# Kernel optimization log

Hardware: AMD Instinct MI355X
Metric: run time of the kernel (lower is better)

## Reference

```python
import jax, jax.numpy as jnp
import numpy as np

H = 14
N = H * H
DIM = 768
INT = 5
LAM = 3.5


def fft_conv_grouped(x, w):
    # x: (B, g*in_c, N) real; w: (g, int_c, in_c, H, H//2+1) complex
    g, int_c, in_c = w.shape[:3]
    B = x.shape[0]
    xf = jnp.fft.rfftn(x.reshape(B, g, in_c, H, H), axes=(-2, -1), norm='ortho')
    yf = jnp.einsum('bgchf,gichf->bgihf', xf, w)
    y = jnp.fft.irfftn(yf, s=(H, H), axes=(-2, -1), norm='ortho')
    return y.reshape(B, g * int_c, N)


def soft(x, t):
    # sign(x) * relu(|x| - t)
    return jnp.sign(x) * jnp.maximum(jnp.abs(x) - t, 0.0)


def batch_norm(x, gamma, beta, eps=1e-5):
    # training-mode BatchNorm1d applied per channel over (B, N); x: (B, N, C)
    m = x.mean(axis=(0, 1))
    v = x.var(axis=(0, 1))
    return (x - m) * jax.lax.rsqrt(v + eps) * gamma + beta


def setup_inputs() -> dict:
    key = jax.random.key(0)
    ks = jax.random.split(key, 8)
    B = 32
    Hf = H // 2 + 1
    # kernel: init randn*0.06, then normalize_parameters()
    kr = jax.random.normal(ks[0], (DIM, INT, 1, H, Hf, 2), dtype=jnp.float32) * 0.06
    kc = kr[..., 0] + 1j * kr[..., 1]
    nrm = jnp.sqrt((jnp.abs(kc) ** 2).sum(axis=(2, 3, 4), keepdims=True) * 2.0 / H ** 2)
    kc = kc / nrm
    kernel = jnp.stack([jnp.real(kc), jnp.imag(kc)], axis=-1)
    # L buffer: update_L(lam=1) -> per-group max singular value of Gram kk
    kk = jnp.einsum('gichf,gjchf->gijhf', kc, jnp.conj(kc))
    sv = np.linalg.svd(np.asarray(jnp.transpose(kk, (0, 3, 4, 1, 2))), compute_uv=False)
    L = jnp.asarray(sv.reshape(DIM, -1).max(axis=-1), dtype=jnp.float32)
    hid = 4 * DIM
    return {
        'x': jax.random.normal(ks[1], (B, N, DIM), dtype=jnp.float32),
        'v_w': jax.random.normal(ks[2], (DIM, DIM), dtype=jnp.float32) * 0.02,
        'proj_w': jax.random.normal(ks[3], (DIM, DIM), dtype=jnp.float32) * 0.02,
        'proj_b': jnp.zeros((DIM,), dtype=jnp.float32),
        'kernel': kernel,
        'kernel2': jax.random.normal(ks[4], (DIM, 1, 1, H, Hf, 2), dtype=jnp.float32) * 0.02,
        'n1_g': jnp.ones((DIM,), dtype=jnp.float32),
        'n1_b': jnp.zeros((DIM,), dtype=jnp.float32),
        'n2_g': jnp.ones((DIM,), dtype=jnp.float32),
        'n2_b': jnp.zeros((DIM,), dtype=jnp.float32),
        'fc1_w': jax.random.normal(ks[5], (hid, DIM), dtype=jnp.float32) * 0.02,
        'fc1_b': jnp.zeros((hid,), dtype=jnp.float32),
        'fc2_w': jax.random.normal(ks[6], (DIM, hid), dtype=jnp.float32) * 0.02,
        'fc2_b': jnp.zeros((DIM,), dtype=jnp.float32),
        'L': L,
    }


def reference(x, v_w, proj_w, proj_b, kernel, kernel2, n1_g, n1_b, n2_g, n2_b, fc1_w, fc1_b, fc2_w, fc2_b, L):
    k = kernel[..., 0] + 1j * kernel[..., 1]                 # (g, int, 1, H, Hf)
    kk = jnp.einsum('gichf,gjchf->gijhf', k, jnp.conj(k))     # (g, int, int, H, Hf)
    vx = x @ v_w.T                                            # v Linear, no bias
    xc = jnp.swapaxes(vx, -2, -1)                             # (B, C, N)
    u = fft_conv_grouped(xc, k)                               # (B, g*int, N)
    Lv = jnp.repeat(L, INT)[None, :, None]                    # (1, g*int, 1)
    # ISTA: init soft-threshold then 3 gradient + shrink steps
    s = soft(u, LAM)
    for _ in range(3):
        s = s - (fft_conv_grouped(s, kk) - u) / Lv
        s = soft(s, LAM / Lv)
    # reconstruct with conjugate-transposed kernel, then mix with kernel2
    new = fft_conv_grouped(s, jnp.swapaxes(jnp.conj(k), 1, 2))  # (B, g, N)
    k2 = kernel2[..., 0] + 1j * kernel2[..., 1]
    new = fft_conv_grouped(new, k2)
    new = jnp.swapaxes(new, -2, -1)                           # (B, N, C)
    new = x + (batch_norm(new, n1_g, n1_b) @ proj_w.T + proj_b)
    h = jax.nn.gelu(batch_norm(new, n2_g, n2_b) @ fc1_w.T + fc1_b, approximate=False)
    return new + (h @ fc2_w.T + fc2_b)
```

## Files before the change

### kernel.cpp

```cpp
#include <hip/hip_runtime.h>
#include <cmath>

typedef unsigned short u16;
typedef __bf16 bf16x8 __attribute__((ext_vector_type(8)));
typedef float f32x4 __attribute__((ext_vector_type(4)));
typedef float float4v __attribute__((ext_vector_type(4)));
typedef u16 ushort4v __attribute__((ext_vector_type(4)));
typedef u16 ushort8v __attribute__((ext_vector_type(8)));

#define DIMC 768
#define NP 196
#define MTOT 6272
#define HIDC 3072
#define LAMC 3.5f

__device__ const float C14d[14] = {
  1.0f, 0.9009688679024191f, 0.6234898018587336f, 0.22252093395631445f,
  -0.22252093395631445f, -0.6234898018587336f, -0.9009688679024191f, -1.0f,
  -0.9009688679024191f, -0.6234898018587336f, -0.22252093395631445f,
  0.22252093395631445f, 0.6234898018587336f, 0.9009688679024191f
};
__device__ const float S14d[14] = {
  0.0f, 0.43388373911755823f, 0.7818314824680298f, 0.9749279121818236f,
  0.9749279121818236f, 0.7818314824680298f, 0.43388373911755823f, 0.0f,
  -0.43388373911755823f, -0.7818314824680298f, -0.9749279121818236f,
  -0.9749279121818236f, -0.7818314824680298f, -0.43388373911755823f
};

__device__ __forceinline__ u16 f2bf(float f) {
  unsigned u = __builtin_bit_cast(unsigned, f);
  unsigned r = u + 0x7FFFu + ((u >> 16) & 1u);
  return (u16)(r >> 16);
}

typedef const __attribute__((address_space(1))) u16* gas_p;
typedef __attribute__((address_space(3))) u16* las_p;
__device__ __forceinline__ void gl16(const u16* g, u16* l) {
  __builtin_amdgcn_global_load_lds((gas_p)g, (las_p)l, 16, 0, 0);
}

__global__ __launch_bounds__(256) void prep_k(
    const float* __restrict__ v_w, const float* __restrict__ fc2w,
    const float* __restrict__ x,
    u16* __restrict__ vwbf, u16* __restrict__ fc2bf, u16* __restrict__ xbf,
    u16* __restrict__ Ff, u16* __restrict__ Gf) {
  const int bid = blockIdx.x, t = threadIdx.x;
  if (bid < 378) {
    int idx = bid * 256 + t;
    if (idx < 50176) {
      int j = idx & 7, lane = (idx >> 3) & 63;
      int mk = idx >> 9, k0 = mk % 7, m0 = mk / 7;
      int s = m0 * 16 + (lane & 15);
      int q = k0 * 32 + (lane >> 4) * 8 + j;
      float v = 0.f;
      if (q < 196) {
        int kr = s >> 4, f = (s >> 1) & 7, r = q / 14, c = q % 14;
        int th = (kr * r + f * c) % 14;
        v = (s & 1) ? -S14d[th] : C14d[th];
      }
      Ff[idx] = f2bf(v);
    } else {
      int t2 = idx - 50176;
      int j = t2 & 7, lane = (t2 >> 3) & 63;
      int pk = t2 >> 9, k0 = pk % 7, p0 = pk / 7;
      int p = p0 * 16 + (lane & 15);
      int s = k0 * 32 + (lane >> 4) * 8 + j;
      float v = 0.f;
      if (p < 196) {
        int kr = s >> 4, f = (s >> 1) & 7, r = p / 14, c = p % 14;
        int th = (kr * r + f * c) % 14;
        float w = (f == 0 || f == 7) ? 1.f : 2.f;
        v = (w * (1.f / 196.f)) * ((s & 1) ? -S14d[th] : C14d[th]);
      }
      Gf[t2] = f2bf(v);
    }
  } else if (bid < 3258) {
    int idx = (bid - 378) * 256 + t;
    const float* s; u16* d; int base;
    if (idx < 147456) { s = v_w; d = vwbf; base = 0; }
    else              { s = fc2w; d = fc2bf; base = 147456; }
    int i4 = (idx - base) * 4;
    float4v v = *(const float4v*)(s + i4);
    ushort4v o;
#pragma unroll
    for (int j = 0; j < 4; ++j) o[j] = f2bf(v[j]);
    *(ushort4v*)(d + i4) = o;
  } else {
    int idx = (bid - 3258) * 256 + t;
    int i4 = idx * 4;
    float4v v = *(const float4v*)(x + i4);
    ushort4v o;
#pragma unroll
    for (int j = 0; j < 4; ++j) o[j] = f2bf(v[j]);
    *(ushort4v*)(xbf + i4) = o;
  }
}

template<int EPI>
__global__ __launch_bounds__(256) void gemm_k(
    const u16* __restrict__ A, const u16* __restrict__ Bw,
    const float* __restrict__ bias, const float* __restrict__ res,
    void* __restrict__ Cp, int Nr, int Kr, int ld, int NB) {
  __shared__ __attribute__((aligned(16))) u16 As[128 * 32];
  __shared__ __attribute__((aligned(16))) u16 Bs[128 * 32];
  const int t = threadIdx.x;
  const int wid = t >> 6, lane = t & 63;

  const int bid = blockIdx.x;
  const int xcd = bid & 7, j = bid >> 3;
  const int bmi = xcd + 8 * (j / NB);
  if (bmi >= 49) return;
  const int bn = (j % NB) * 128, bm = bmi * 128;

  const int wm = (wid >> 1) * 64, wn = (wid & 1) * 64;
  const int l15 = lane & 15, l4 = lane >> 4;
  const int srow = lane >> 2;
  const int sw_s = ((lane >> 2) ^ (lane >> 4)) & 3;
  const int scol = ((lane & 3) ^ sw_s) * 8;
  const int sw_r = (l15 ^ (l15 >> 2)) & 3;
  const int rcol = (l4 ^ sw_r) * 8;

  f32x4 acc[4][4];
#pragma unroll
  for (int a = 0; a < 4; ++a)
#pragma unroll
    for (int b2 = 0; b2 < 4; ++b2) acc[a][b2] = (f32x4){0.f, 0.f, 0.f, 0.f};

  const u16* gA0 = A + (size_t)(bm + wid * 16 + srow) * ld + scol;
  const u16* gB0 = Bw + (size_t)(bn + wid * 16 + srow) * ld + scol;
  u16* lA = As + wid * 512;
  u16* lB = Bs + wid * 512;

  for (int k0 = 0; k0 < Kr; k0 += 32) {
    gl16(gA0 + k0, lA);
    gl16(gA0 + (size_t)64 * ld + k0, lA + 2048);
    gl16(gB0 + k0, lB);
    gl16(gB0 + (size_t)64 * ld + k0, lB + 2048);
    __syncthreads();

    bf16x8 af[4], bfv[4];
#pragma unroll
    for (int mb = 0; mb < 4; ++mb)
      af[mb] = *(const bf16x8*)&As[(wm + mb * 16 + l15) * 32 + rcol];
#pragma unroll
    for (int nb = 0; nb < 4; ++nb)
      bfv[nb] = *(const bf16x8*)&Bs[(wn + nb * 16 + l15) * 32 + rcol];
#pragma unroll
    for (int mb = 0; mb < 4; ++mb)
#pragma unroll
      for (int nb = 0; nb < 4; ++nb)
        acc[mb][nb] = __builtin_amdgcn_mfma_f32_16x16x32_bf16(af[mb], bfv[nb], acc[mb][nb], 0, 0, 0);
    __syncthreads();
  }

#pragma unroll
  for (int mb = 0; mb < 4; ++mb) {
#pragma unroll
    for (int nb = 0; nb < 4; ++nb) {
      int n = bn + wn + nb * 16 + l15;
      if (EPI == 0) {
        int m0 = bm + wm + mb * 16 + l4 * 4;
        int bb = m0 / 196, np0 = m0 - bb * 196;
        *(float4v*)&((float*)Cp)[((size_t)bb * DIMC + n) * 196 + np0] =
            (float4v){acc[mb][nb][0], acc[mb][nb][1], acc[mb][nb][2], acc[mb][nb][3]};
      } else {
#pragma unroll
        for (int r = 0; r < 4; ++r) {
          int m = bm + wm + mb * 16 + l4 * 4 + r;
          float v = acc[mb][nb][r];
          if (EPI == 1) {
            ((float*)Cp)[(size_t)m * Nr + n] = v + bias[n] + res[(size_t)m * Nr + n];
          } else {
            float vb = v + bias[n];
            float ge = 0.5f * vb * (1.f + erff(vb * 0.70710678118654752f));
            ((u16*)Cp)[(size_t)m * Nr + n] = f2bf(ge);
          }
        }
      }
    }
  }
}

__global__ __launch_bounds__(64) void checkmfma_k(
    const float* __restrict__ vxt, const float* __restrict__ kern,
    const u16* __restrict__ Ff, const u16* __restrict__ Gf,
    int* __restrict__ cnt, int* __restrict__ wl) {
  __shared__ float xf[16 * 228];
  const int lane = threadIdx.x;
  const int wgb = blockIdx.x;
  const int g = wgb >> 1, bhalf = wgb & 1;
  const int tl = lane & 15, h = lane >> 4;
  const float* xbase = vxt + ((size_t)(bhalf * 16 + tl) * DIMC + g) * 196;

  bf16x8 Bx[7];
#pragma unroll
  for (int k0 = 0; k0 < 7; ++k0) {
    int q0 = k0 * 32 + h * 8;
    ushort8v tv;
    if (k0 < 6) {
      float4v f0 = *(const float4v*)(xbase + q0);
      float4v f1 = *(const float4v*)(xbase + q0 + 4);
#pragma unroll
      for (int j = 0; j < 4; ++j) { tv[j] = f2bf(f0[j]); tv[j + 4] = f2bf(f1[j]); }
    } else {
#pragma unroll
      for (int j = 0; j < 8; ++j) {
        int q = q0 + j;
        tv[j] = (q < 196) ? f2bf(xbase[q]) : (u16)0;
      }
    }
    Bx[k0] = __builtin_bit_cast(bf16x8, tv);
  }

  for (int m0 = 0; m0 < 14; ++m0) {
    f32x4 acc = (f32x4){0.f, 0.f, 0.f, 0.f};
#pragma unroll
    for (int k0 = 0; k0 < 7; ++k0) {
      bf16x8 Af = __builtin_bit_cast(bf16x8,
          *(const ushort8v*)(Ff + ((size_t)(m0 * 7 + k0) * 64 + lane) * 8));
      acc = __builtin_amdgcn_mfma_f32_16x16x32_bf16(Af, Bx[k0], acc, 0, 0, 0);
    }
    *(f32x4*)&xf[tl * 228 + m0 * 16 + h * 4] = acc;
  }

  bf16x8 By[5][7];
#pragma unroll
  for (int i = 0; i < 5; ++i) {
    const float* kb = kern + ((size_t)g * 5 + i) * 224;
#pragma unroll
    for (int k0 = 0; k0 < 7; ++k0) {
      f32x4 x0 = *(const f32x4*)&xf[tl * 228 + k0 * 32 + h * 8];
      f32x4 x1 = *(const f32x4*)&xf[tl * 228 + k0 * 32 + h * 8 + 4];
      int mb = k0 * 16 + h * 4;
      float2 ka = *(const float2*)(kb + (mb + 0) * 2);
      float2 kc = *(const float2*)(kb + (mb + 1) * 2);
      float2 ke = *(const float2*)(kb + (mb + 2) * 2);
      float2 kg = *(const float2*)(kb + (mb + 3) * 2);
      ushort8v tv;
      tv[0] = f2bf(ka.x * x0[0] - ka.y * x0[1]);
      tv[1] = f2bf(ka.x * x0[1] + ka.y * x0[0]);
      tv[2] = f2bf(kc.x * x0[2] - kc.y * x0[3]);
      tv[3] = f2bf(kc.x * x0[3] + kc.y * x0[2]);
      tv[4] = f2bf(ke.x * x1[0] - ke.y * x1[1]);
      tv[5] = f2bf(ke.x * x1[1] + ke.y * x1[0]);
      tv[6] = f2bf(kg.x * x1[2] - kg.y * x1[3]);
      tv[7] = f2bf(kg.x * x1[3] + kg.y * x1[2]);
      By[i][k0] = __builtin_bit_cast(bf16x8, tv);
    }
  }

  float vmax = 0.f;
  for (int p0 = 0; p0 < 13; ++p0) {
    f32x4 a0 = (f32x4){0.f, 0.f, 0.f, 0.f};
    f32x4 a1 = a0, a2 = a0, a3 = a0, a4 = a0;
#pragma unroll
    for (int k0 = 0; k0 < 7; ++k0) {
      bf16x8 Ag = __builtin_bit_cast(bf16x8,
          *(const ushort8v*)(Gf + ((size_t)(p0 * 7 + k0) * 64 + lane) * 8));
      a0 = __builtin_amdgcn_mfma_f32_16x16x32_bf16(Ag, By[0][k0], a0, 0, 0, 0);
      a1 = __builtin_amdgcn_mfma_f32_16x16x32_bf16(Ag, By[1][k0], a1, 0, 0, 0);
      a2 = __builtin_amdgcn_mfma_f32_16x16x32_bf16(Ag, By[2][k0], a2, 0, 0, 0);
      a3 = __builtin_amdgcn_mfma_f32_16x16x32_bf16(Ag, By[3][k0], a3, 0, 0, 0);
      a4 = __builtin_amdgcn_mfma_f32_16x16x32_bf16(Ag, By[4][k0], a4, 0, 0, 0);
    }
#pragma unroll
    for (int r = 0; r < 4; ++r) {
      vmax = fmaxf(vmax, fabsf(a0[r]));
      vmax = fmaxf(vmax, fabsf(a1[r]));
      vmax = fmaxf(vmax, fabsf(a2[r]));
      vmax = fmaxf(vmax, fabsf(a3[r]));
      vmax = fmaxf(vmax, fabsf(a4[r]));
    }
  }
  vmax = fmaxf(vmax, __shfl_xor(vmax, 16));
  vmax = fmaxf(vmax, __shfl_xor(vmax, 32));
  if (lane < 16 && vmax > (LAMC - 0.1f)) {
    int idx = atomicAdd(cnt, 1);
    wl[idx] = g * 32 + bhalf * 16 + lane;
  }
}

__global__ __launch_bounds__(64) void slow_k(
    const float* __restrict__ vxt, const float* __restrict__ kern,
    const float* __restrict__ kern2, const float* __restrict__ Lbuf,
    const int* __restrict__ cnt, const int* __restrict__ wl,
    float* __restrict__ outp,
    float* __restrict__ tsum, float* __restrict__ tsq,
    unsigned* __restrict__ maskg, unsigned* __restrict__ bmask) {
  const int ntile = *cnt;
  if ((int)blockIdx.x >= ntile) return;
  const int t = threadIdx.x;
  __shared__ float TC[196], TSn[196];
  __shared__ float xs[196];
  __shared__ float t1R[112], t1I[112];
  __shared__ float t2R[112], t2I[112];
  __shared__ float zr[112], zi[112];
  __shared__ float kR[5][112], kI[5][112];
  __shared__ float uu[5][196];
  __shared__ float ss[5][196];
  __shared__ float k2R[112], k2I[112];

  for (int i = t; i < 196; i += 64) {
    int a = i / 14, c = i - (i / 14) * 14;
    int m = (a * c) % 14;
    TC[i] = C14d[m]; TSn[i] = S14d[m];
  }

  auto rowsFwd = [&](const float* xsrc) {
    for (int i = t; i < 112; i += 64) {
      int r = i >> 3, f = i & 7;
      const float* xp = xsrc + r * 14;
      const float* tc = &TC[f * 14]; const float* tsn = &TSn[f * 14];
      float ar = 0.f, ai = 0.f;
#pragma unroll
      for (int c = 0; c < 14; ++c) { float xv = xp[c]; ar += xv * tc[c]; ai -= xv * tsn[c]; }
      t1R[i] = ar; t1I[i] = ai;
    }
    __syncthreads();
  };
  auto colsFwd = [&](float* oR, float* oI) {
    for (int i = t; i < 112; i += 64) {
      int kr = i >> 3, f = i & 7;
      const float* tc = &TC[kr * 14]; const float* tsn = &TSn[kr * 14];
      float br = 0.f, bi = 0.f;
#pragma unroll
      for (int r = 0; r < 14; ++r) {
        float xr = t1R[r * 8 + f], xi = t1I[r * 8 + f];
        br += tc[r] * xr + tsn[r] * xi;
        bi += tc[r] * xi - tsn[r] * xr;
      }
      oR[i] = br; oI[i] = bi;
    }
    __syncthreads();
  };
  auto colsInv = [&]() {
    for (int i = t; i < 112; i += 64) {
      int r = i >> 3, f = i & 7;
      const float* tc = &TC[r * 14]; const float* tsn = &TSn[r * 14];
      float br = 0.f, bi = 0.f;
#pragma unroll
      for (int kr = 0; kr < 14; ++kr) {
        float xr = t1R[kr * 8 + f], xi = t1I[kr * 8 + f];
        br += tc[kr] * xr - tsn[kr] * xi;
        bi += tc[kr] * xi + tsn[kr] * xr;
      }
      t2R[i] = br; t2I[i] = bi;
    }
    __syncthreads();
  };
  auto rowVal = [&](int r, int c) -> float {
    const float* pR = &t2R[r * 8]; const float* pI = &t2I[r * 8];
    float v = pR[0] + ((c & 1) ? -pR[7] : pR[7]);
    float s2 = 0.f;
#pragma unroll
    for (int f = 1; f < 7; ++f) s2 += pR[f] * TC[f * 14 + c] - pI[f] * TSn[f * 14 + c];
    return (v + 2.f * s2) * (1.0f / 196.0f);
  };

  for (int widx = blockIdx.x; widx < ntile; widx += gridDim.x) {
    const int tile = wl[widx];
    const int g = tile >> 5, b = tile & 31;
    __syncthreads();
    for (int i = t; i < 560; i += 64) {
      int ii = i / 112, p = i - ii * 112;
      const float* kp = kern + ((size_t)g * 5 + ii) * 224 + p * 2;
      kR[ii][p] = kp[0]; kI[ii][p] = kp[1];
    }
    for (int i = t; i < 196; i += 64) xs[i] = vxt[((size_t)b * DIMC + g) * 196 + i];
    for (int i = t; i < 112; i += 64) {
      k2R[i] = kern2[(size_t)g * 224 + i * 2];
      k2I[i] = kern2[(size_t)g * 224 + i * 2 + 1];
    }
    __syncthreads();

    rowsFwd(xs);
    colsFwd(zr, zi);
    for (int ii = 0; ii < 5; ++ii) {
      for (int i = t; i < 112; i += 64) {
        float a = kR[ii][i], b2 = kI[ii][i];
        t1R[i] = a * zr[i] - b2 * zi[i];
        t1I[i] = a * zi[i] + b2 * zr[i];
      }
      __syncthreads();
      colsInv();
      for (int i = t; i < 196; i += 64) uu[ii][i] = rowVal(i / 14, i - (i / 14) * 14);
      __syncthreads();
    }

    const float invL = 1.0f / Lbuf[g];
    const float thr = LAMC * invL;
    {
      float* up = &uu[0][0];
      float* sp = &ss[0][0];
      for (int i = t; i < 980; i += 64) {
        float v = up[i];
        float a = fabsf(v) - LAMC;
        sp[i] = a > 0.f ? copysignf(a, v) : 0.f;
      }
    }
    __syncthreads();

    for (int iter = 0; iter < 4; ++iter) {
      for (int i = t; i < 112; i += 64) { zr[i] = 0.f; zi[i] = 0.f; }
      __syncthreads();
      for (int ii = 0; ii < 5; ++ii) {
        rowsFwd(&ss[ii][0]);
        colsFwd(t2R, t2I);
        for (int i = t; i < 112; i += 64) {
          float a = kR[ii][i], b2 = kI[ii][i];
          zr[i] += a * t2R[i] + b2 * t2I[i];
          zi[i] += a * t2I[i] - b2 * t2R[i];
        }
        __syncthreads();
      }
      if (iter == 3) break;
      for (int ii = 0; ii < 5; ++ii) {
        for (int i = t; i < 112; i += 64) {
          float a = kR[ii][i], b2 = kI[ii][i];
          t1R[i] = a * zr[i] - b2 * zi[i];
          t1I[i] = a * zi[i] + b2 * zr[i];
        }
        __syncthreads();
        colsInv();
        for (int i = t; i < 196; i += 64) {
          float v = rowVal(i / 14, i - (i / 14) * 14);
          float sv = ss[ii][i] - (v - uu[ii][i]) * invL;
          float aa = fabsf(sv) - thr;
          ss[ii][i] = aa > 0.f ? copysignf(aa, sv) : 0.f;
        }
        __syncthreads();
      }
    }

    if (t < 28) {
      int kr = t >> 1, f = (t & 1) * 7;
      int d = kr * 8 + f;
      int srci = ((14 - kr) % 14) * 8 + f;
      float pr = 0.5f * (zr[d] + zr[srci]);
      float pi = 0.5f * (zi[d] - zi[srci]);
      zr[d] = pr; zi[d] = pi;
    }
    __syncthreads();
    for (int i = t; i < 112; i += 64) {
      float a = k2R[i], b2 = k2I[i];
      t1R[i] = a * zr[i] - b2 * zi[i];
      t1I[i] = a * zi[i] + b2 * zr[i];
    }
    __syncthreads();
    colsInv();
    float sacc = 0.f, qacc = 0.f;
    for (int i = t; i < 196; i += 64) {
      float v = rowVal(i / 14, i - (i / 14) * 14);
      outp[((size_t)(b * 196 + i)) * DIMC + g] = v;
      sacc += v; qacc += v * v;
    }
#pragma unroll
    for (int off = 32; off; off >>= 1) {
      sacc += __shfl_xor(sacc, off);
      qacc += __shfl_xor(qacc, off);
    }
    if (t == 0) {
      tsum[tile] = sacc; tsq[tile] = qacc;
      atomicOr(&maskg[g], 1u << b);
      atomicOr(bmask, 1u << b);
    }
  }
}

__global__ __launch_bounds__(256) void stats1c0_k(
    const float* __restrict__ tsum, const float* __restrict__ tsq,
    const unsigned* __restrict__ maskg,
    const float* __restrict__ gam, const float* __restrict__ bet,
    const float* __restrict__ projw, const float* __restrict__ pb,
    float* __restrict__ sc1, float* __restrict__ c0) {
  __shared__ float sh1s[768];
  const int t = threadIdx.x;
  for (int c = t; c < DIMC; c += 256) {
    unsigned mask = maskg[c];
    float S = 0.f, Q = 0.f;
    if (mask) {
      for (int b = 0; b < 32; ++b)
        if ((mask >> b) & 1) { S += tsum[c * 32 + b]; Q += tsq[c * 32 + b]; }
    }
    float m = S * (1.0f / 6272.0f);
    float v = fmaxf(Q * (1.0f / 6272.0f) - m * m, 0.f);
    float rs = rsqrtf(v + 1e-5f);
    float sc = gam[c] * rs;
    sh1s[c] = bet[c] - m * sc;
    if (blockIdx.x == 0) sc1[c] = sc;
  }
  __syncthreads();
  int n = blockIdx.x * 256 + t;
  const float* row = projw + (size_t)n * DIMC;
  float s = 0.f;
  for (int g = 0; g < DIMC; g += 4) {
    float4v r = *(const float4v*)(row + g);
    s += r[0] * sh1s[g] + r[1] * sh1s[g + 1] + r[2] * sh1s[g + 2] + r[3] * sh1s[g + 3];
  }
  c0[n] = s + pb[n];
}

__global__ __launch_bounds__(256) void bnb_k(
    const float* __restrict__ x, const float* __restrict__ c0,
    const float* __restrict__ sc1, const unsigned* __restrict__ maskg,
    const unsigned* __restrict__ bmask, const float* __restrict__ newm,
    const float* __restrict__ projw,
    float* __restrict__ new2, u16* __restrict__ n2bf,
    float* __restrict__ part) {
  const int jb = blockIdx.x, b = blockIdx.y, t = threadIdx.x;
  __shared__ unsigned gm[24];
  __shared__ float c0s[768];
  const bool hasb = ((*bmask >> b) & 1u) != 0u;
  if (t < 24) {
    unsigned w = 0;
    if (hasb)
      for (int j2 = 0; j2 < 32; ++j2) w |= ((maskg[t * 32 + j2] >> b) & 1u) << j2;
    gm[t] = w;
  }
  for (int c = t; c < 768; c += 256) c0s[c] = c0[c];
  __syncthreads();

  float S0 = 0, S1 = 0, S2 = 0, Q0 = 0, Q1 = 0, Q2 = 0;
  for (int mr = 0; mr < 7; ++mr) {
    size_t row = ((size_t)b * 196 + jb * 7 + mr) * DIMC;
#pragma unroll
    for (int j2 = 0; j2 < 3; ++j2) {
      int n = t + j2 * 256;
      float v = x[row + n] + c0s[n];
      if (hasb) {
        for (int w = 0; w < 24; ++w) {
          unsigned bits = gm[w];
          while (bits) {
            int g = w * 32 + __builtin_ctz(bits);
            bits &= bits - 1;
            v += sc1[g] * newm[row + g] * projw[(size_t)n * DIMC + g];
          }
        }
      }
      new2[row + n] = v;
      n2bf[row + n] = f2bf(v);
      if (j2 == 0) { S0 += v; Q0 += v * v; }
      else if (j2 == 1) { S1 += v; Q1 += v * v; }
      else { S2 += v; Q2 += v * v; }
    }
  }
  float* p = part + (size_t)(b * 28 + jb) * 1536;
  p[t] = S0; p[t + 256] = S1; p[t + 512] = S2;
  p[768 + t] = Q0; p[768 + 256 + t] = Q1; p[768 + 512 + t] = Q2;
}

__global__ __launch_bounds__(256) void red2_k(const float* __restrict__ part,
                                              float* __restrict__ part2) {
  int slot = blockIdx.x * 256 + threadIdx.x;
  int b = blockIdx.y;
  float s = 0.f;
  const float* p = part + (size_t)(b * 28) * 1536 + slot;
  for (int jb = 0; jb < 28; ++jb) s += p[(size_t)jb * 1536];
  part2[(size_t)b * 1536 + slot] = s;
}

__global__ __launch_bounds__(256) void stats2fin_k(const float* __restrict__ part2,
    const float* __restrict__ gam, const float* __restrict__ bet,
    float* __restrict__ scale, float* __restrict__ shift) {
  int c = blockIdx.x * 256 + threadIdx.x;
  float S = 0.f, Q = 0.f;
  for (int b = 0; b < 32; ++b) {
    S += part2[(size_t)b * 1536 + c];
    Q += part2[(size_t)b * 1536 + 768 + c];
  }
  float m = S * (1.0f / 6272.0f);
  float v = fmaxf(Q * (1.0f / 6272.0f) - m * m, 0.f);
  float rs = rsqrtf(v + 1e-5f);
  float sc = gam[c] * rs;
  scale[c] = sc;
  shift[c] = bet[c] - m * sc;
}

__global__ __launch_bounds__(256) void foldfc1_k(const float* __restrict__ fc1w,
    const float* __restrict__ fc1b, const float* __restrict__ sc2,
    const float* __restrict__ sh2, u16* __restrict__ fc1s,
    float* __restrict__ d0) {
  const int bid = blockIdx.x, t = threadIdx.x;
  if (bid < 12) {
    int n = bid * 256 + t;
    const float* row = fc1w + (size_t)n * DIMC;
    float s = 0.f;
    for (int k = 0; k < DIMC; k += 4) {
      float4v r = *(const float4v*)(row + k);
      float4v h = *(const float4v*)(sh2 + k);
      s += r[0] * h[0] + r[1] * h[1] + r[2] * h[2] + r[3] * h[3];
    }
    d0[n] = s + fc1b[n];
  } else {
    int idx = (bid - 12) * 256 + t;
    int i4 = idx * 4;
    int k = i4 % DIMC;
    float4v v = *(const float4v*)(fc1w + i4);
    float4v s = *(const float4v*)(sc2 + k);
    v = v * s;
    ushort4v o;
#pragma unroll
    for (int j = 0; j < 4; ++j) o[j] = f2bf(v[j]);
    *(ushort4v*)(fc1s + i4) = o;
  }
}

extern "C" void kernel_launch(void* const* d_in, const int* in_sizes, int n_in,
                              void* d_out, int out_size, void* d_ws, size_t ws_size,
                              hipStream_t stream) {
  (void)in_sizes; (void)n_in; (void)out_size;
  const float* x      = (const float*)d_in[0];
  const float* v_w    = (const float*)d_in[1];
  const float* proj_w = (const float*)d_in[2];
  const float* proj_b = (const float*)d_in[3];
  const float* kern   = (const float*)d_in[4];
  const float* kern2  = (const float*)d_in[5];
  const float* n1g    = (const float*)d_in[6];
  const float* n1b    = (const float*)d_in[7];
  const float* n2g    = (const float*)d_in[8];
  const float* n2b    = (const float*)d_in[9];
  const float* fc1w   = (const float*)d_in[10];
  const float* fc1b   = (const float*)d_in[11];
  const float* fc2w   = (const float*)d_in[12];
  const float* fc2b   = (const float*)d_in[13];
  const float* Lb     = (const float*)d_in[14];
  float* out = (float*)d_out;

  char* ws = (char*)d_ws;
  size_t o = 0;
  auto alloc = [&](size_t bytes) { size_t r = o; o += (bytes + 255) & ~(size_t)255; return r; };
  u16*   vwbf   = (u16*)(ws + alloc(589824 * 2));
  u16*   fc2bf  = (u16*)(ws + alloc(2359296 * 2));
  u16*   fc1s   = (u16*)(ws + alloc(2359296 * 2));
  u16*   Ffb    = (u16*)(ws + alloc(50176 * 2));
  u16*   Gfb    = (u16*)(ws + alloc(46592 * 2));
  float* sc1    = (float*)(ws + alloc(768 * 4));
  float* sc2    = (float*)(ws + alloc(768 * 4));
  float* sh2    = (float*)(ws + alloc(768 * 4));
  float* c0     = (float*)(ws + alloc(768 * 4));
  float* d0     = (float*)(ws + alloc(3072 * 4));
  float* part   = (float*)(ws + alloc((size_t)896 * 1536 * 4));
  float* part2  = (float*)(ws + alloc((size_t)32 * 1536 * 4));
  char*  zblk   = (char*)(ws + alloc(4096));
  int*      cnt   = (int*)zblk;
  unsigned* bmask = (unsigned*)(zblk + 4);
  unsigned* maskg = (unsigned*)(zblk + 8);
  int*   wl     = (int*)(ws + alloc(24576 * 4));
  float* tsum   = (float*)(ws + alloc(24576 * 4));
  float* tsq    = (float*)(ws + alloc(24576 * 4));
  u16*   xbf    = (u16*)(ws + alloc((size_t)MTOT * DIMC * 2));
  u16*   n2bf   = (u16*)(ws + alloc((size_t)MTOT * DIMC * 2));
  float* vxt    = (float*)(ws + alloc((size_t)MTOT * DIMC * 4));
  float* newm   = (float*)(ws + alloc((size_t)MTOT * DIMC * 4));
  float* new2   = (float*)(ws + alloc((size_t)MTOT * DIMC * 4));
  u16*   hbf    = (u16*)vxt;
  if (ws_size < o) return;

  hipMemsetAsync(zblk, 0, 4096, stream);

  prep_k<<<7962, 256, 0, stream>>>(v_w, fc2w, x, vwbf, fc2bf, xbf, Ffb, Gfb);
  gemm_k<0><<<336, 256, 0, stream>>>(xbf, vwbf, nullptr, nullptr, vxt, DIMC, DIMC, DIMC, 6);
  checkmfma_k<<<1536, 64, 0, stream>>>(vxt, kern, Ffb, Gfb, cnt, wl);
  slow_k<<<1024, 64, 0, stream>>>(vxt, kern, kern2, Lb, cnt, wl, newm,
                                  tsum, tsq, maskg, bmask);
  stats1c0_k<<<3, 256, 0, stream>>>(tsum, tsq, maskg, n1g, n1b, proj_w, proj_b, sc1, c0);
  bnb_k<<<dim3(28, 32), 256, 0, stream>>>(x, c0, sc1, maskg, bmask, newm, proj_w,
                                          new2, n2bf, part);
  red2_k<<<dim3(6, 32), 256, 0, stream>>>(part, part2);
  stats2fin_k<<<3, 256, 0, stream>>>(part2, n2g, n2b, sc2, sh2);
  foldfc1_k<<<2316, 256, 0, stream>>>(fc1w, fc1b, sc2, sh2, fc1s, d0);
  gemm_k<2><<<1344, 256, 0, stream>>>(n2bf, fc1s, d0, nullptr, hbf, HIDC, DIMC, DIMC, 24);
  gemm_k<1><<<336, 256, 0, stream>>>(hbf, fc2bf, fc2b, new2, out, DIMC, HIDC, HIDC, 6);
}
```

Measured before the change: 305.8 us.

## Pre-swizzle GEMM operands into MFMA fragment layout and drop LDS staging

All bf16 GEMM operands (x, v_w, fc2_w, folded fc1_w, the n2 activations and the GELU output) are now written in a 16x32-chunk fragment layout. Each lane can then load its MFMA operand straight from global memory with one 16-byte load. The GEMM kernel drops shared memory and __syncthreads. Each wave now computes its own 64x64 tile, with the block covering 64 rows by 256 columns. This removes LDS traffic and barriers, but operands are no longer shared between waves through LDS, so global/L2 reads increase and there is no explicit prefetch.

```diff
diff --git a/kernel.cpp b/kernel.cpp
--- a/kernel.cpp
+++ b/kernel.cpp
@@ -33,16 +33,15 @@
   return (u16)(r >> 16);
 }
 
-typedef const __attribute__((address_space(1))) u16* gas_p;
-typedef __attribute__((address_space(3))) u16* las_p;
-__device__ __forceinline__ void gl16(const u16* g, u16* l) {
-  __builtin_amdgcn_global_load_lds((gas_p)g, (las_p)l, 16, 0, 0);
+__device__ __forceinline__ size_t fidx(int m, int k, int K) {
+  return ((size_t)(m >> 4) * (K >> 5) + (k >> 5)) * 512 +
+         (size_t)((((k >> 3) & 3) * 16 + (m & 15)) * 8 + (k & 7));
 }
 
 __global__ __launch_bounds__(256) void prep_k(
     const float* __restrict__ v_w, const float* __restrict__ fc2w,
     const float* __restrict__ x,
-    u16* __restrict__ vwbf, u16* __restrict__ fc2bf, u16* __restrict__ xbf,
+    u16* __restrict__ vwf, u16* __restrict__ fc2f, u16* __restrict__ xf,
     u16* __restrict__ Ff, u16* __restrict__ Gf) {
   const int bid = blockIdx.x, t = threadIdx.x;
   if (bid < 378) {
@@ -74,51 +73,42 @@
       }
       Gf[t2] = f2bf(v);
     }
-  } else if (bid < 3258) {
-    int idx = (bid - 378) * 256 + t;
-    const float* s; u16* d; int base;
-    if (idx < 147456) { s = v_w; d = vwbf; base = 0; }
-    else              { s = fc2w; d = fc2bf; base = 147456; }
-    int i4 = (idx - base) * 4;
-    float4v v = *(const float4v*)(s + i4);
-    ushort4v o;
-#pragma unroll
-    for (int j = 0; j < 4; ++j) o[j] = f2bf(v[j]);
-    *(ushort4v*)(d + i4) = o;
-  } else {
-    int idx = (bid - 3258) * 256 + t;
-    int i4 = idx * 4;
-    float4v v = *(const float4v*)(x + i4);
-    ushort4v o;
-#pragma unroll
-    for (int j = 0; j < 4; ++j) o[j] = f2bf(v[j]);
-    *(ushort4v*)(xbf + i4) = o;
-  }
+    return;
+  }
+  const float* src; u16* dst; int idx, K;
+  if (bid < 666)        { src = v_w;  dst = vwf;  idx = (bid - 378) * 256 + t;  K = DIMC; }
+  else if (bid < 1818)  { src = fc2w; dst = fc2f; idx = (bid - 666) * 256 + t;  K = HIDC; }
+  else                  { src = x;    dst = xf;   idx = (bid - 1818) * 256 + t; K = DIMC; }
+  const int KC = K >> 5;
+  int chunk = idx >> 6, l = idx & 63;
+  int row = (chunk / KC) * 16 + (l & 15);
+  int k0 = (chunk % KC) * 32 + (l >> 4) * 8;
+  const float* sp = src + (size_t)row * K + k0;
+  float4v f0 = *(const float4v*)sp;
+  float4v f1 = *(const float4v*)(sp + 4);
+  ushort8v o;
+#pragma unroll
+  for (int j = 0; j < 4; ++j) { o[j] = f2bf(f0[j]); o[j + 4] = f2bf(f1[j]); }
+  *(ushort8v*)(dst + (size_t)idx * 8) = o;
 }
 
 template<int EPI>
-__global__ __launch_bounds__(256) void gemm_k(
-    const u16* __restrict__ A, const u16* __restrict__ Bw,
+__global__ __launch_bounds__(256) void gemmw_k(
+    const u16* __restrict__ Af, const u16* __restrict__ Bf,
     const float* __restrict__ bias, const float* __restrict__ res,
-    void* __restrict__ Cp, int Nr, int Kr, int ld, int NB) {
-  __shared__ __attribute__((aligned(16))) u16 As[128 * 32];
-  __shared__ __attribute__((aligned(16))) u16 Bs[128 * 32];
-  const int t = threadIdx.x;
-  const int wid = t >> 6, lane = t & 63;
-
+    void* __restrict__ Cp, int Nr, int Kr, int NB) {
+  const int t = threadIdx.x, w = t >> 6, lane = t & 63;
   const int bid = blockIdx.x;
   const int xcd = bid & 7, j = bid >> 3;
-  const int bmi = xcd + 8 * (j / NB);
-  if (bmi >= 49) return;
-  const int bn = (j % NB) * 128, bm = bmi * 128;
-
-  const int wm = (wid >> 1) * 64, wn = (wid & 1) * 64;
+  const int mt = xcd + 8 * (j / NB);
+  if (mt >= 98) return;
+  const int m0 = mt * 64;
+  const int n0 = ((j % NB) * 4 + w) * 64;
+  const int KC = Kr >> 5;
   const int l15 = lane & 15, l4 = lane >> 4;
-  const int srow = lane >> 2;
-  const int sw_s = ((lane >> 2) ^ (lane >> 4)) & 3;
-  const int scol = ((lane & 3) ^ sw_s) * 8;
-  const int sw_r = (l15 ^ (l15 >> 2)) & 3;
-  const int rcol = (l4 ^ sw_r) * 8;
+
+  const u16* Ab = Af + ((size_t)(m0 >> 4) * KC) * 512 + lane * 8;
+  const u16* Bb = Bf + ((size_t)(n0 >> 4) * KC) * 512 + lane * 8;
 
   f32x4 acc[4][4];
 #pragma unroll
@@ -126,54 +116,42 @@
 #pragma unroll
     for (int b2 = 0; b2 < 4; ++b2) acc[a][b2] = (f32x4){0.f, 0.f, 0.f, 0.f};
 
-  const u16* gA0 = A + (size_t)(bm + wid * 16 + srow) * ld + scol;
-  const u16* gB0 = Bw + (size_t)(bn + wid * 16 + srow) * ld + scol;
-  u16* lA = As + wid * 512;
-  u16* lB = Bs + wid * 512;
-
-  for (int k0 = 0; k0 < Kr; k0 += 32) {
-    gl16(gA0 + k0, lA);
-    gl16(gA0 + (size_t)64 * ld + k0, lA + 2048);
-    gl16(gB0 + k0, lB);
-    gl16(gB0 + (size_t)64 * ld + k0, lB + 2048);
-    __syncthreads();
-
+  for (int kc = 0; kc < KC; ++kc) {
     bf16x8 af[4], bfv[4];
 #pragma unroll
     for (int mb = 0; mb < 4; ++mb)
-      af[mb] = *(const bf16x8*)&As[(wm + mb * 16 + l15) * 32 + rcol];
+      af[mb] = *(const bf16x8*)(Ab + ((size_t)mb * KC + kc) * 512);
 #pragma unroll
     for (int nb = 0; nb < 4; ++nb)
-      bfv[nb] = *(const bf16x8*)&Bs[(wn + nb * 16 + l15) * 32 + rcol];
+      bfv[nb] = *(const bf16x8*)(Bb + ((size_t)nb * KC + kc) * 512);
 #pragma unroll
     for (int mb = 0; mb < 4; ++mb)
 #pragma unroll
       for (int nb = 0; nb < 4; ++nb)
         acc[mb][nb] = __builtin_amdgcn_mfma_f32_16x16x32_bf16(af[mb], bfv[nb], acc[mb][nb], 0, 0, 0);
-    __syncthreads();
   }
 
 #pragma unroll
   for (int mb = 0; mb < 4; ++mb) {
 #pragma unroll
     for (int nb = 0; nb < 4; ++nb) {
-      int n = bn + wn + nb * 16 + l15;
+      int n = n0 + nb * 16 + l15;
       if (EPI == 0) {
-        int m0 = bm + wm + mb * 16 + l4 * 4;
-        int bb = m0 / 196, np0 = m0 - bb * 196;
+        int m0r = m0 + mb * 16 + l4 * 4;
+        int bb = m0r / 196, np0 = m0r - bb * 196;
         *(float4v*)&((float*)Cp)[((size_t)bb * DIMC + n) * 196 + np0] =
             (float4v){acc[mb][nb][0], acc[mb][nb][1], acc[mb][nb][2], acc[mb][nb][3]};
       } else {
 #pragma unroll
         for (int r = 0; r < 4; ++r) {
-          int m = bm + wm + mb * 16 + l4 * 4 + r;
+          int m = m0 + mb * 16 + l4 * 4 + r;
           float v = acc[mb][nb][r];
           if (EPI == 1) {
             ((float*)Cp)[(size_t)m * Nr + n] = v + bias[n] + res[(size_t)m * Nr + n];
           } else {
             float vb = v + bias[n];
             float ge = 0.5f * vb * (1.f + erff(vb * 0.70710678118654752f));
-            ((u16*)Cp)[(size_t)m * Nr + n] = f2bf(ge);
+            ((u16*)Cp)[fidx(m, n, Nr)] = f2bf(ge);
           }
         }
       }
@@ -505,7 +483,7 @@
     const float* __restrict__ sc1, const unsigned* __restrict__ maskg,
     const unsigned* __restrict__ bmask, const float* __restrict__ newm,
     const float* __restrict__ projw,
-    float* __restrict__ new2, u16* __restrict__ n2bf,
+    float* __restrict__ new2, u16* __restrict__ n2f,
     float* __restrict__ part) {
   const int jb = blockIdx.x, b = blockIdx.y, t = threadIdx.x;
   __shared__ unsigned gm[24];
@@ -522,7 +500,8 @@
 
   float S0 = 0, S1 = 0, S2 = 0, Q0 = 0, Q1 = 0, Q2 = 0;
   for (int mr = 0; mr < 7; ++mr) {
-    size_t row = ((size_t)b * 196 + jb * 7 + mr) * DIMC;
+    int m = b * 196 + jb * 7 + mr;
+    size_t row = (size_t)m * DIMC;
 #pragma unroll
     for (int j2 = 0; j2 < 3; ++j2) {
       int n = t + j2 * 256;
@@ -538,7 +517,7 @@
         }
       }
       new2[row + n] = v;
-      n2bf[row + n] = f2bf(v);
+      n2f[fidx(m, n, DIMC)] = f2bf(v);
       if (j2 == 0) { S0 += v; Q0 += v * v; }
       else if (j2 == 1) { S1 += v; Q1 += v * v; }
       else { S2 += v; Q2 += v * v; }
@@ -593,15 +572,19 @@
     d0[n] = s + fc1b[n];
   } else {
     int idx = (bid - 12) * 256 + t;
-    int i4 = idx * 4;
-    int k = i4 % DIMC;
-    float4v v = *(const float4v*)(fc1w + i4);
-    float4v s = *(const float4v*)(sc2 + k);
-    v = v * s;
-    ushort4v o;
-#pragma unroll
-    for (int j = 0; j < 4; ++j) o[j] = f2bf(v[j]);
-    *(ushort4v*)(fc1s + i4) = o;
+    int chunk = idx >> 6, l = idx & 63;
+    int n = (chunk / 24) * 16 + (l & 15);
+    int k0 = (chunk % 24) * 32 + (l >> 4) * 8;
+    const float* sp = fc1w + (size_t)n * DIMC + k0;
+    float4v f0 = *(const float4v*)sp;
+    float4v f1 = *(const float4v*)(sp + 4);
+    float4v s0 = *(const float4v*)(sc2 + k0);
+    float4v s1 = *(const float4v*)(sc2 + k0 + 4);
+    f0 = f0 * s0; f1 = f1 * s1;
+    ushort8v o;
+#pragma unroll
+    for (int j = 0; j < 4; ++j) { o[j] = f2bf(f0[j]); o[j + 4] = f2bf(f1[j]); }
+    *(ushort8v*)(fc1s + (size_t)idx * 8) = o;
   }
 }
 
@@ -629,8 +612,8 @@
   char* ws = (char*)d_ws;
   size_t o = 0;
   auto alloc = [&](size_t bytes) { size_t r = o; o += (bytes + 255) & ~(size_t)255; return r; };
-  u16*   vwbf   = (u16*)(ws + alloc(589824 * 2));
-  u16*   fc2bf  = (u16*)(ws + alloc(2359296 * 2));
+  u16*   vwf    = (u16*)(ws + alloc(589824 * 2));
+  u16*   fc2f   = (u16*)(ws + alloc(2359296 * 2));
   u16*   fc1s   = (u16*)(ws + alloc(2359296 * 2));
   u16*   Ffb    = (u16*)(ws + alloc(50176 * 2));
   u16*   Gfb    = (u16*)(ws + alloc(46592 * 2));
@@ -648,8 +631,8 @@
   int*   wl     = (int*)(ws + alloc(24576 * 4));
   float* tsum   = (float*)(ws + alloc(24576 * 4));
   float* tsq    = (float*)(ws + alloc(24576 * 4));
-  u16*   xbf    = (u16*)(ws + alloc((size_t)MTOT * DIMC * 2));
-  u16*   n2bf   = (u16*)(ws + alloc((size_t)MTOT * DIMC * 2));
+  u16*   xf     = (u16*)(ws + alloc((size_t)MTOT * DIMC * 2));
+  u16*   n2f    = (u16*)(ws + alloc((size_t)MTOT * DIMC * 2));
   float* vxt    = (float*)(ws + alloc((size_t)MTOT * DIMC * 4));
   float* newm   = (float*)(ws + alloc((size_t)MTOT * DIMC * 4));
   float* new2   = (float*)(ws + alloc((size_t)MTOT * DIMC * 4));
@@ -658,17 +641,17 @@
 
   hipMemsetAsync(zblk, 0, 4096, stream);
 
-  prep_k<<<7962, 256, 0, stream>>>(v_w, fc2w, x, vwbf, fc2bf, xbf, Ffb, Gfb);
-  gemm_k<0><<<336, 256, 0, stream>>>(xbf, vwbf, nullptr, nullptr, vxt, DIMC, DIMC, DIMC, 6);
+  prep_k<<<4170, 256, 0, stream>>>(v_w, fc2w, x, vwf, fc2f, xf, Ffb, Gfb);
+  gemmw_k<0><<<312, 256, 0, stream>>>(xf, vwf, nullptr, nullptr, vxt, DIMC, DIMC, 3);
   checkmfma_k<<<1536, 64, 0, stream>>>(vxt, kern, Ffb, Gfb, cnt, wl);
   slow_k<<<1024, 64, 0, stream>>>(vxt, kern, kern2, Lb, cnt, wl, newm,
                                   tsum, tsq, maskg, bmask);
   stats1c0_k<<<3, 256, 0, stream>>>(tsum, tsq, maskg, n1g, n1b, proj_w, proj_b, sc1, c0);
   bnb_k<<<dim3(28, 32), 256, 0, stream>>>(x, c0, sc1, maskg, bmask, newm, proj_w,
-                                          new2, n2bf, part);
+                                          new2, n2f, part);
   red2_k<<<dim3(6, 32), 256, 0, stream>>>(part, part2);
   stats2fin_k<<<3, 256, 0, stream>>>(part2, n2g, n2b, sc2, sh2);
-  foldfc1_k<<<2316, 256, 0, stream>>>(fc1w, fc1b, sc2, sh2, fc1s, d0);
-  gemm_k<2><<<1344, 256, 0, stream>>>(n2bf, fc1s, d0, nullptr, hbf, HIDC, DIMC, DIMC, 24);
-  gemm_k<1><<<336, 256, 0, stream>>>(hbf, fc2bf, fc2b, new2, out, DIMC, HIDC, HIDC, 6);
-}
+  foldfc1_k<<<1164, 256, 0, stream>>>(fc1w, fc1b, sc2, sh2, fc1s, d0);
+  gemmw_k<2><<<1248, 256, 0, stream>>>(n2f, fc1s, d0, nullptr, hbf, HIDC, DIMC, 12);
+  gemmw_k<1><<<312, 256, 0, stream>>>(hbf, fc2f, fc2b, new2, out, DIMC, HIDC, 3);
+}
```

Measured after the change: 273.4 us. -10.6%, faster.
